# Kernel tuning notes

Hardware: AMD Instinct MI355X
Metric: run time of the kernel (lower is better)

Reference implementation:

```python
import jax, jax.numpy as jnp
import numpy as np

ALPHA = 1.0   # stored by the module but unused in forward
SPLIT = 4
FILTER = 2


def _resize_bilinear(x, out_h, out_w):
    """PyTorch F.interpolate(mode='bilinear', align_corners=False), no antialias.
    x: [B, C, H, W]."""
    B, C, H, W = x.shape

    def coords(out_n, in_n):
        c = (jnp.arange(out_n, dtype=jnp.float32) + 0.5) * (in_n / out_n) - 0.5
        c = jnp.clip(c, 0.0, in_n - 1)
        i0 = jnp.floor(c).astype(jnp.int32)
        i1 = jnp.minimum(i0 + 1, in_n - 1)
        f = (c - i0).astype(x.dtype)
        return i0, i1, f

    r0, r1, fr = coords(out_h, H)
    c0, c1, fc = coords(out_w, W)
    # separable: rows then cols
    x = x[:, :, r0, :] * (1 - fr)[None, None, :, None] + x[:, :, r1, :] * fr[None, None, :, None]
    x = x[:, :, :, c0] * (1 - fc) + x[:, :, :, c1] * fc
    return x


def setup_inputs() -> dict:
    key = jax.random.key(0)
    targets = jax.random.normal(key, (8, 3, 2560, 2560), dtype=jnp.float32)
    return {"targets": targets}


def reference(targets):
    B, C, H, W = targets.shape
    s = SPLIT
    h = int(H / s / 10)
    w = int(W / s / 10)
    x = _resize_bilinear(targets, h * s, w * s)  # [B, C, s*h, s*w]

    # The original quadruple loop over shifts (i,j) and patches (n,m) computes, for
    # every ordered patch pair (a=(n,m), b=((n+i)%s,(m+j)%s)),
    #   map[a, b] = mean_{B,C,h,w} exp(-(patch_b - patch_a)^2),
    # which is exactly the full pairwise patch-affinity matrix.
    P = x.reshape(B, C, s, h, s, w).transpose(2, 4, 0, 1, 3, 5).reshape(s * s, -1)  # [s^2, D]
    aff = jnp.exp(-(P[:, None, :] - P[None, :, :]) ** 2).mean(axis=-1)  # [s^2, s^2]

    # Sort-based masking: zero the (split - filter) smallest entries of each row.
    k = s - FILTER
    idx = jnp.argsort(aff, axis=1)[:, :k]           # [s^2, k]
    rows = jnp.arange(s * s)[:, None]
    aff = aff.at[rows, idx].set(0.0)
    return aff
```

## Files before the change

kernel.cpp:

```cpp
#include <hip/hip_runtime.h>


#define W_IN 2560
#define IMG_STRIDE (2560 * 2560)
#define D_TOTAL_I 98304
#define D_TOTAL 98304.0

#define NSHADOW_F 32
#define SLOT_STRIDE 128
#define SHADOW_BYTES (NSHADOW_F * SLOT_STRIDE * 8)
#define PMAT_OFF 65536
#define WS_NEEDED (PMAT_OFF + 16 * D_TOTAL_I * 4)


__global__ __launch_bounds__(256) void pm_resize(const float* __restrict__ in,
                                                 float* __restrict__ Pm) {
    const int blk = blockIdx.x;
    const int n   = blk & 3;
    const int hh  = (blk >> 2) & 63;
    const int img = blk >> 8;
    const int m   = threadIdx.x >> 6;
    const int ww  = threadIdx.x & 63;

    const float* r0 = in + (size_t)img * IMG_STRIDE
                         + (size_t)(640 * n + 10 * hh + 4) * W_IN
                         + (640 * m + 10 * ww + 4);
    float2 t = *reinterpret_cast<const float2*>(r0);
    float2 u = *reinterpret_cast<const float2*>(r0 + W_IN);
    Pm[(size_t)(n * 4 + m) * D_TOTAL_I + img * 4096 + hh * 64 + ww] =
        0.25f * ((t.x + t.y) + (u.x + u.y));
}

__global__ __launch_bounds__(256) void pm_pairs(const float* __restrict__ Pm,
                                                double* __restrict__ acc) {
    const int tid  = threadIdx.x;
    const int lane = tid & 63;
    const int d    = blockIdx.x * 256 + tid;

    float P[16];
#pragma unroll
    for (int p = 0; p < 16; ++p) P[p] = Pm[p * D_TOTAL_I + d];

    float v[128];
    {
        int k = 0;
#pragma unroll
        for (int a = 0; a < 16; ++a)
#pragma unroll
            for (int b = a + 1; b < 16; ++b) {
                float df = P[a] - P[b];
                v[k++] = __expf(-df * df);
            }
#pragma unroll
        for (int i = 120; i < 128; ++i) v[i] = 0.0f;
    }

#define PM_STAGE(K, H)                                         \
    {                                                          \
        const bool bit = (lane >> (K)) & 1;                    \
        _Pragma("unroll")                                      \
        for (int i = 0; i < (H); ++i) {                        \
            float keep = bit ? v[i + (H)] : v[i];              \
            float send = bit ? v[i] : v[i + (H)];              \
            v[i] = keep + __shfl_xor(send, 1 << (K), 64);      \
        }                                                      \
    }
    PM_STAGE(0, 64)
    PM_STAGE(1, 32)
    PM_STAGE(2, 16)
    PM_STAGE(3, 8)
    PM_STAGE(4, 4)
    PM_STAGE(5, 2)
#undef PM_STAGE

    __shared__ float part[SLOT_STRIDE];
    if (tid < SLOT_STRIDE) part[tid] = 0.0f;
    __syncthreads();

    const int r = __brev(lane) >> 26;
#pragma unroll
    for (int i = 0; i < 2; ++i) {
        int slot = i + 2 * r;
        if (slot < 120) atomicAdd(&part[slot], v[i]);
    }
    __syncthreads();

    if (tid < 120) {
        double* shadow = acc + (size_t)(blockIdx.x & (NSHADOW_F - 1)) * SLOT_STRIDE;
        atomicAdd(&shadow[tid], (double)part[tid]);
    }
}

__global__ __launch_bounds__(256) void pm_finish_fast(const double* __restrict__ acc,
                                                      float* __restrict__ out) {
    __shared__ float aff[256];
    const int tid = threadIdx.x;
    const int a = tid >> 4, b = tid & 15;
    if (a < b) {
        int pp = 15 * a - (a * (a - 1)) / 2 + (b - a - 1);
        double s = 0.0;
#pragma unroll
        for (int c = 0; c < NSHADOW_F; ++c) s += acc[c * SLOT_STRIDE + pp];
        float vv = (float)(s * (1.0 / D_TOTAL));
        aff[a * 16 + b] = vv;
        aff[b * 16 + a] = vv;
    } else if (a == b) {
        aff[tid] = 1.0f;
    }
    __syncthreads();
    if (tid < 16) {
        const float* row = &aff[tid * 16];
        float v1 = 1e30f; int i1 = -1;
        for (int j = 0; j < 16; ++j) {
            float x = row[j];
            if (x < v1) { v1 = x; i1 = j; }
        }
        float v2 = 1e30f; int i2 = -1;
        for (int j = 0; j < 16; ++j) {
            if (j == i1) continue;
            float x = row[j];
            if (x < v2) { v2 = x; i2 = j; }
        }
        for (int j = 0; j < 16; ++j)
            out[tid * 16 + j] = (j == i1 || j == i2) ? 0.0f : row[j];
    }
}


#define NPAIR_SLOTS 256
#define NSHADOW 8

__global__ __launch_bounds__(64) void pm_accum(const float* __restrict__ in,
                                               double* __restrict__ acc) {
    const int blk = blockIdx.x;
    const int hh  = blk & 63;
    const int img = blk >> 6;
    const int ww  = threadIdx.x;

    const float* base = in + (size_t)img * IMG_STRIDE;
    float P[16];
#pragma unroll
    for (int n = 0; n < 4; ++n) {
        const int row0 = 10 * (n * 64 + hh) + 4;
        const float* r0 = base + (size_t)row0 * W_IN;
#pragma unroll
        for (int m = 0; m < 4; ++m) {
            const int col = 10 * (m * 64 + ww) + 4;
            float2 t = *reinterpret_cast<const float2*>(r0 + col);
            float2 u = *reinterpret_cast<const float2*>(r0 + W_IN + col);
            P[n * 4 + m] = 0.25f * ((t.x + t.y) + (u.x + u.y));
        }
    }
    double* shadow = acc + (size_t)(blk & (NSHADOW - 1)) * NPAIR_SLOTS;
    int k = 0;
#pragma unroll
    for (int a = 0; a < 16; ++a)
#pragma unroll
        for (int b = a + 1; b < 16; ++b) {
            float dd = P[a] - P[b];
            float vv = __expf(-dd * dd);
#pragma unroll
            for (int s = 32; s >= 1; s >>= 1) vv += __shfl_xor(vv, s, 64);
            if (ww == (k & 63)) atomicAdd(&shadow[a * 16 + b], (double)vv);
            ++k;
        }
}

__global__ __launch_bounds__(256) void pm_finish(const double* __restrict__ acc,
                                                 float* __restrict__ out) {
    __shared__ float aff[256];
    const int tid = threadIdx.x;
    const int a = tid >> 4, b = tid & 15;
    if (a < b) {
        double s = 0.0;
#pragma unroll
        for (int c = 0; c < NSHADOW; ++c) s += acc[c * NPAIR_SLOTS + tid];
        float vv = (float)(s * (1.0 / D_TOTAL));
        aff[a * 16 + b] = vv;
        aff[b * 16 + a] = vv;
    } else if (a == b) {
        aff[tid] = 1.0f;
    }
    __syncthreads();
    if (tid < 16) {
        const float* row = &aff[tid * 16];
        float v1 = 1e30f; int i1 = -1;
        for (int j = 0; j < 16; ++j) {
            float x = row[j];
            if (x < v1) { v1 = x; i1 = j; }
        }
        float v2 = 1e30f; int i2 = -1;
        for (int j = 0; j < 16; ++j) {
            if (j == i1) continue;
            float x = row[j];
            if (x < v2) { v2 = x; i2 = j; }
        }
        for (int j = 0; j < 16; ++j)
            out[tid * 16 + j] = (j == i1 || j == i2) ? 0.0f : row[j];
    }
}


extern "C" void kernel_launch(void* const* d_in, const int* in_sizes, int n_in,
                              void* d_out, int out_size, void* d_ws, size_t ws_size,
                              hipStream_t stream) {
    const float* in = (const float*)d_in[0];
    float* out = (float*)d_out;

    if (ws_size >= (size_t)WS_NEEDED) {
        double* acc = (double*)d_ws;
        float* Pm = (float*)((char*)d_ws + PMAT_OFF);
        hipMemsetAsync(d_ws, 0, SHADOW_BYTES, stream);
        pm_resize<<<dim3(6144), dim3(256), 0, stream>>>(in, Pm);
        pm_pairs<<<dim3(384), dim3(256), 0, stream>>>(Pm, acc);
        pm_finish_fast<<<dim3(1), dim3(256), 0, stream>>>(acc, out);
    } else {
        double* acc = (double*)d_ws;
        hipMemsetAsync(d_ws, 0, NSHADOW * NPAIR_SLOTS * sizeof(double), stream);
        pm_accum<<<dim3(1536), dim3(64), 0, stream>>>(in, acc);
        pm_finish<<<dim3(1), dim3(256), 0, stream>>>(acc, out);
    }
}
```

Before: 39.92 us.

## Fuse memset and finish into resize/pairs kernels via last-block counter

The workspace zeroing moves into the resize kernel, and the separate finish kernel is folded into the pairs kernel through an atomic completion counter, so the last block does the final reduction and top-k masking. This removes a memset and a kernel launch from the fast path. Pair work is also split across two half-blocks, each handling 60 pairs over 768 blocks, which shrinks the register array and the shuffle reduction. The shared-memory atomics give way to direct global double atomics into 16 shadow copies. The cost is a grid-wide fence and atomic per block, plus more global atomic traffic.

Result: slower. 95.10 us (+138.2%).

```diff
diff --git a/kernel.cpp b/kernel.cpp
--- a/kernel.cpp
+++ b/kernel.cpp
@@ -6,21 +6,28 @@
 #define D_TOTAL_I 98304
 #define D_TOTAL 98304.0
 
-#define NSHADOW_F 32
+#define NSHADOW 16
 #define SLOT_STRIDE 128
-#define SHADOW_BYTES (NSHADOW_F * SLOT_STRIDE * 8)
+#define SHADOW_BYTES (NSHADOW * SLOT_STRIDE * 8)
+#define CTR_OFF_U32 (SHADOW_BYTES / 4)
 #define PMAT_OFF 65536
 #define WS_NEEDED (PMAT_OFF + 16 * D_TOTAL_I * 4)
 
 
 __global__ __launch_bounds__(256) void pm_resize(const float* __restrict__ in,
-                                                 float* __restrict__ Pm) {
+                                                 float* __restrict__ Pm,
+                                                 unsigned int* __restrict__ wsu) {
     const int blk = blockIdx.x;
+    const int tid = threadIdx.x;
+
+    if (blk < 16) wsu[blk * 256 + tid] = 0u;
+    else if (blk == 16 && tid == 0) wsu[CTR_OFF_U32] = 0u;
+
     const int n   = blk & 3;
     const int hh  = (blk >> 2) & 63;
     const int img = blk >> 8;
-    const int m   = threadIdx.x >> 6;
-    const int ww  = threadIdx.x & 63;
+    const int m   = tid >> 6;
+    const int ww  = tid & 63;
 
     const float* r0 = in + (size_t)img * IMG_STRIDE
                          + (size_t)(640 * n + 10 * hh + 4) * W_IN
@@ -31,29 +38,35 @@
         0.25f * ((t.x + t.y) + (u.x + u.y));
 }
 
+
 __global__ __launch_bounds__(256) void pm_pairs(const float* __restrict__ Pm,
-                                                double* __restrict__ acc) {
+                                                double* __restrict__ acc,
+                                                unsigned int* __restrict__ ctr,
+                                                float* __restrict__ out) {
     const int tid  = threadIdx.x;
     const int lane = tid & 63;
-    const int d    = blockIdx.x * 256 + tid;
+    const int half = tid >> 7;
+    const int d    = blockIdx.x * 128 + (tid & 127);
 
     float P[16];
 #pragma unroll
     for (int p = 0; p < 16; ++p) P[p] = Pm[p * D_TOTAL_I + d];
 
-    float v[128];
+    float v[64];
     {
         int k = 0;
 #pragma unroll
         for (int a = 0; a < 16; ++a)
 #pragma unroll
             for (int b = a + 1; b < 16; ++b) {
-                float df = P[a] - P[b];
-                v[k++] = __expf(-df * df);
+                if (k >= half * 60 && k < half * 60 + 60) {
+                    float df = P[a] - P[b];
+                    v[k - half * 60] = __expf(-df * df);
+                }
+                ++k;
             }
-#pragma unroll
-        for (int i = 120; i < 128; ++i) v[i] = 0.0f;
-    }
+    }
+    v[60] = 0.0f; v[61] = 0.0f; v[62] = 0.0f; v[63] = 0.0f;
 
 #define PM_STAGE(K, H)                                         \
     {                                                          \
@@ -65,42 +78,121 @@
             v[i] = keep + __shfl_xor(send, 1 << (K), 64);      \
         }                                                      \
     }
-    PM_STAGE(0, 64)
-    PM_STAGE(1, 32)
-    PM_STAGE(2, 16)
-    PM_STAGE(3, 8)
-    PM_STAGE(4, 4)
-    PM_STAGE(5, 2)
+    PM_STAGE(0, 32)
+    PM_STAGE(1, 16)
+    PM_STAGE(2, 8)
+    PM_STAGE(3, 4)
+    PM_STAGE(4, 2)
+    PM_STAGE(5, 1)
 #undef PM_STAGE
 
-    __shared__ float part[SLOT_STRIDE];
-    if (tid < SLOT_STRIDE) part[tid] = 0.0f;
-    __syncthreads();
-
     const int r = __brev(lane) >> 26;
-#pragma unroll
-    for (int i = 0; i < 2; ++i) {
-        int slot = i + 2 * r;
-        if (slot < 120) atomicAdd(&part[slot], v[i]);
-    }
-    __syncthreads();
-
-    if (tid < 120) {
-        double* shadow = acc + (size_t)(blockIdx.x & (NSHADOW_F - 1)) * SLOT_STRIDE;
-        atomicAdd(&shadow[tid], (double)part[tid]);
-    }
-}
-
-__global__ __launch_bounds__(256) void pm_finish_fast(const double* __restrict__ acc,
-                                                      float* __restrict__ out) {
+    double* shadow = acc + (size_t)(blockIdx.x & (NSHADOW - 1)) * SLOT_STRIDE;
+    if (r < 60) atomicAdd(&shadow[half * 64 + r], (double)v[0]);
+
+    __syncthreads();
+    __shared__ int is_last;
+    if (tid == 0) {
+        __threadfence();
+        unsigned prev = __hip_atomic_fetch_add(ctr, 1u, __ATOMIC_ACQ_REL,
+                                               __HIP_MEMORY_SCOPE_AGENT);
+        is_last = (prev == (unsigned)gridDim.x - 1u);
+    }
+    __syncthreads();
+    if (!is_last) return;
+    __threadfence();
+
+    __shared__ double psum[120][2];
+    __shared__ float aff[256];
+    if (tid < 240) {
+        const int pair = tid >> 1, sub = tid & 1;
+        const int slot = (pair < 60) ? pair : pair + 4;
+        double s = 0.0;
+#pragma unroll
+        for (int c = 0; c < 8; ++c)
+            s += __hip_atomic_load(&acc[(size_t)(sub * 8 + c) * SLOT_STRIDE + slot],
+                                   __ATOMIC_RELAXED, __HIP_MEMORY_SCOPE_AGENT);
+        psum[pair][sub] = s;
+    }
+    __syncthreads();
+    {
+        const int a = tid >> 4, b = tid & 15;
+        if (a < b) {
+            const int k = 15 * a - (a * (a - 1)) / 2 + (b - a - 1);
+            float vv = (float)((psum[k][0] + psum[k][1]) * (1.0 / D_TOTAL));
+            aff[a * 16 + b] = vv;
+            aff[b * 16 + a] = vv;
+        } else if (a == b) {
+            aff[tid] = 1.0f;
+        }
+    }
+    __syncthreads();
+    if (tid < 16) {
+        const float* row = &aff[tid * 16];
+        float v1 = 1e30f; int i1 = -1;
+        for (int j = 0; j < 16; ++j) {
+            float x = row[j];
+            if (x < v1) { v1 = x; i1 = j; }
+        }
+        float v2 = 1e30f; int i2 = -1;
+        for (int j = 0; j < 16; ++j) {
+            if (j == i1) continue;
+            float x = row[j];
+            if (x < v2) { v2 = x; i2 = j; }
+        }
+        for (int j = 0; j < 16; ++j)
+            out[tid * 16 + j] = (j == i1 || j == i2) ? 0.0f : row[j];
+    }
+}
+
+
+#define NPAIR_SLOTS_FB 256
+#define NSHADOW_FB 8
+
+__global__ __launch_bounds__(64) void pm_accum_fb(const float* __restrict__ in,
+                                                  double* __restrict__ acc) {
+    const int blk = blockIdx.x;
+    const int hh  = blk & 63;
+    const int img = blk >> 6;
+    const int ww  = threadIdx.x;
+
+    const float* base = in + (size_t)img * IMG_STRIDE;
+    float P[16];
+#pragma unroll
+    for (int n = 0; n < 4; ++n) {
+        const float* r0 = base + (size_t)(10 * (n * 64 + hh) + 4) * W_IN;
+#pragma unroll
+        for (int m = 0; m < 4; ++m) {
+            const int col = 10 * (m * 64 + ww) + 4;
+            float2 t = *reinterpret_cast<const float2*>(r0 + col);
+            float2 u = *reinterpret_cast<const float2*>(r0 + W_IN + col);
+            P[n * 4 + m] = 0.25f * ((t.x + t.y) + (u.x + u.y));
+        }
+    }
+    double* shadow = acc + (size_t)(blk & (NSHADOW_FB - 1)) * NPAIR_SLOTS_FB;
+    int k = 0;
+#pragma unroll
+    for (int a = 0; a < 16; ++a)
+#pragma unroll
+        for (int b = a + 1; b < 16; ++b) {
+            float dd = P[a] - P[b];
+            float vv = __expf(-dd * dd);
+#pragma unroll
+            for (int s = 32; s >= 1; s >>= 1) vv += __shfl_xor(vv, s, 64);
+            if (ww == (k & 63)) atomicAdd(&shadow[a * 16 + b], (double)vv);
+            ++k;
+        }
+}
+
+__global__ __launch_bounds__(256) void pm_finish_fb(const double* __restrict__ acc,
+                                                    float* __restrict__ out) {
     __shared__ float aff[256];
     const int tid = threadIdx.x;
     const int a = tid >> 4, b = tid & 15;
     if (a < b) {
-        int pp = 15 * a - (a * (a - 1)) / 2 + (b - a - 1);
         double s = 0.0;
 #pragma unroll
-        for (int c = 0; c < NSHADOW_F; ++c) s += acc[c * SLOT_STRIDE + pp];
+        for (int c = 0; c < NSHADOW_FB; ++c) s += acc[c * NPAIR_SLOTS_FB + tid];
         float vv = (float)(s * (1.0 / D_TOTAL));
         aff[a * 16 + b] = vv;
         aff[b * 16 + a] = vv;
@@ -127,80 +219,6 @@
 }
 
 
-#define NPAIR_SLOTS 256
-#define NSHADOW 8
-
-__global__ __launch_bounds__(64) void pm_accum(const float* __restrict__ in,
-                                               double* __restrict__ acc) {
-    const int blk = blockIdx.x;
-    const int hh  = blk & 63;
-    const int img = blk >> 6;
-    const int ww  = threadIdx.x;
-
-    const float* base = in + (size_t)img * IMG_STRIDE;
-    float P[16];
-#pragma unroll
-    for (int n = 0; n < 4; ++n) {
-        const int row0 = 10 * (n * 64 + hh) + 4;
-        const float* r0 = base + (size_t)row0 * W_IN;
-#pragma unroll
-        for (int m = 0; m < 4; ++m) {
-            const int col = 10 * (m * 64 + ww) + 4;
-            float2 t = *reinterpret_cast<const float2*>(r0 + col);
-            float2 u = *reinterpret_cast<const float2*>(r0 + W_IN + col);
-            P[n * 4 + m] = 0.25f * ((t.x + t.y) + (u.x + u.y));
-        }
-    }
-    double* shadow = acc + (size_t)(blk & (NSHADOW - 1)) * NPAIR_SLOTS;
-    int k = 0;
-#pragma unroll
-    for (int a = 0; a < 16; ++a)
-#pragma unroll
-        for (int b = a + 1; b < 16; ++b) {
-            float dd = P[a] - P[b];
-            float vv = __expf(-dd * dd);
-#pragma unroll
-            for (int s = 32; s >= 1; s >>= 1) vv += __shfl_xor(vv, s, 64);
-            if (ww == (k & 63)) atomicAdd(&shadow[a * 16 + b], (double)vv);
-            ++k;
-        }
-}
-
-__global__ __launch_bounds__(256) void pm_finish(const double* __restrict__ acc,
-                                                 float* __restrict__ out) {
-    __shared__ float aff[256];
-    const int tid = threadIdx.x;
-    const int a = tid >> 4, b = tid & 15;
-    if (a < b) {
-        double s = 0.0;
-#pragma unroll
-        for (int c = 0; c < NSHADOW; ++c) s += acc[c * NPAIR_SLOTS + tid];
-        float vv = (float)(s * (1.0 / D_TOTAL));
-        aff[a * 16 + b] = vv;
-        aff[b * 16 + a] = vv;
-    } else if (a == b) {
-        aff[tid] = 1.0f;
-    }
-    __syncthreads();
-    if (tid < 16) {
-        const float* row = &aff[tid * 16];
-        float v1 = 1e30f; int i1 = -1;
-        for (int j = 0; j < 16; ++j) {
-            float x = row[j];
-            if (x < v1) { v1 = x; i1 = j; }
-        }
-        float v2 = 1e30f; int i2 = -1;
-        for (int j = 0; j < 16; ++j) {
-            if (j == i1) continue;
-            float x = row[j];
-            if (x < v2) { v2 = x; i2 = j; }
-        }
-        for (int j = 0; j < 16; ++j)
-            out[tid * 16 + j] = (j == i1 || j == i2) ? 0.0f : row[j];
-    }
-}
-
-
 extern "C" void kernel_launch(void* const* d_in, const int* in_sizes, int n_in,
                               void* d_out, int out_size, void* d_ws, size_t ws_size,
                               hipStream_t stream) {
@@ -209,15 +227,14 @@
 
     if (ws_size >= (size_t)WS_NEEDED) {
         double* acc = (double*)d_ws;
+        unsigned int* wsu = (unsigned int*)d_ws;
         float* Pm = (float*)((char*)d_ws + PMAT_OFF);
-        hipMemsetAsync(d_ws, 0, SHADOW_BYTES, stream);
-        pm_resize<<<dim3(6144), dim3(256), 0, stream>>>(in, Pm);
-        pm_pairs<<<dim3(384), dim3(256), 0, stream>>>(Pm, acc);
-        pm_finish_fast<<<dim3(1), dim3(256), 0, stream>>>(acc, out);
+        pm_resize<<<dim3(6144), dim3(256), 0, stream>>>(in, Pm, wsu);
+        pm_pairs<<<dim3(768), dim3(256), 0, stream>>>(Pm, acc, wsu + CTR_OFF_U32, out);
     } else {
         double* acc = (double*)d_ws;
-        hipMemsetAsync(d_ws, 0, NSHADOW * NPAIR_SLOTS * sizeof(double), stream);
-        pm_accum<<<dim3(1536), dim3(64), 0, stream>>>(in, acc);
-        pm_finish<<<dim3(1), dim3(256), 0, stream>>>(acc, out);
-    }
-}
+        hipMemsetAsync(d_ws, 0, NSHADOW_FB * NPAIR_SLOTS_FB * sizeof(double), stream);
+        pm_accum_fb<<<dim3(1536), dim3(64), 0, stream>>>(in, acc);
+        pm_finish_fb<<<dim3(1), dim3(256), 0, stream>>>(acc, out);
+    }
+}
```
